# Performance work log

Measured on AMD Instinct MI355X. Metric: run time of the kernel, lower is better.

## Reference

```python
import jax, jax.numpy as jnp
import numpy as np

MEM_DIM = 1024
N_CHILD = 16384

def _linear_params(key, out_dim, in_dim):
    kw, kb = jax.random.split(key)
    bound = 1.0 / np.sqrt(in_dim)
    W = jax.random.uniform(kw, (out_dim, in_dim), jnp.float32, -bound, bound)
    b = jax.random.uniform(kb, (out_dim,), jnp.float32, -bound, bound)
    return W, b

def setup_inputs() -> dict:
    key = jax.random.key(0)
    ks = jax.random.split(key, 7)
    child_c = jax.random.normal(ks[0], (N_CHILD, MEM_DIM), jnp.float32)
    child_h = jax.random.normal(ks[1], (N_CHILD, MEM_DIM), jnp.float32)
    child_h_sum = jax.random.normal(ks[2], (MEM_DIM,), jnp.float32)
    W_ih, b_ih = _linear_params(ks[3], MEM_DIM, MEM_DIM)
    W_fh, b_fh = _linear_params(ks[4], MEM_DIM, MEM_DIM)
    W_uh, b_uh = _linear_params(ks[5], MEM_DIM, MEM_DIM)
    W_oh, b_oh = _linear_params(ks[6], MEM_DIM, MEM_DIM)
    return {
        "child_c": child_c, "child_h": child_h, "child_h_sum": child_h_sum,
        "W_ih": W_ih, "b_ih": b_ih, "W_fh": W_fh, "b_fh": b_fh,
        "W_uh": W_uh, "b_uh": b_uh, "W_oh": W_oh, "b_oh": b_oh,
    }

def reference(child_c, child_h, child_h_sum,
              W_ih, b_ih, W_fh, b_fh, W_uh, b_uh, W_oh, b_oh):
    # Gate projections on the summed child hidden state: [mem_dim]
    i = jax.nn.sigmoid(child_h_sum @ W_ih.T + b_ih)
    o = jax.nn.sigmoid(child_h_sum @ W_oh.T + b_oh)
    u = jnp.tanh(child_h_sum @ W_uh.T + b_uh)
    # Per-child forget gates, batched (replaces the Python loop): [N, mem_dim]
    f = jax.nn.sigmoid(child_h @ W_fh.T + b_fh)
    fc = f * child_c                     # [N, mem_dim]
    c = i * u + jnp.sum(fc, axis=0)      # [mem_dim]
    h = o * jnp.tanh(c)                  # [mem_dim]
    return (c, h)
```

## Files before the change

### kernel.cpp

```cpp
#include <hip/hip_runtime.h>
#include <hip/hip_bf16.h>
#include <math.h>

#define MEM_DIM 1024
#define N_CHILD 16384

#define BM 128
#define BN 128
#define BK 32
#define KITERS (MEM_DIM / BK)

typedef __bf16 bf16_t;
typedef __bf16 bf16x4 __attribute__((ext_vector_type(4)));
typedef __bf16 bf16x8 __attribute__((ext_vector_type(8)));
typedef float f32x4 __attribute__((ext_vector_type(4)));

__device__ __forceinline__ int swz(int r) { return (r >> 1) & 3; }

__device__ __forceinline__ void async_load16(const bf16_t* g, bf16_t* l) {
    __builtin_amdgcn_global_load_lds(
        (const __attribute__((address_space(1))) unsigned int*)g,
        (__attribute__((address_space(3))) unsigned int*)l,
        16, 0, 0);
}

__global__ __launch_bounds__(256) void cvt_bf16_kernel(const float* __restrict__ src,
                                                       bf16_t* __restrict__ dst, int n8) {
    int t = blockIdx.x * 256 + threadIdx.x;
    if (t < n8) {
        const float4* s = (const float4*)src + (size_t)t * 2;
        float4 a = s[0], b = s[1];
        bf16x8 o = { (bf16_t)a.x, (bf16_t)a.y, (bf16_t)a.z, (bf16_t)a.w,
                     (bf16_t)b.x, (bf16_t)b.y, (bf16_t)b.z, (bf16_t)b.w };
        *(bf16x8*)(dst + (size_t)t * 8) = o;
    }
}

__global__ void gates_kernel(const float* __restrict__ hsum,
                             const float* __restrict__ W_ih, const float* __restrict__ b_ih,
                             const float* __restrict__ W_uh, const float* __restrict__ b_uh,
                             const float* __restrict__ W_oh, const float* __restrict__ b_oh,
                             float* __restrict__ acc_c, float* __restrict__ o_ws) {
    const int j = blockIdx.x;
    const int tid = threadIdx.x;
    const float* wi = W_ih + (size_t)j * MEM_DIM;
    const float* wu = W_uh + (size_t)j * MEM_DIM;
    const float* wo = W_oh + (size_t)j * MEM_DIM;
    float si = 0.f, su = 0.f, so = 0.f;
    for (int k = tid; k < MEM_DIM; k += 256) {
        float hv = hsum[k];
        si += wi[k] * hv;
        su += wu[k] * hv;
        so += wo[k] * hv;
    }
    for (int off = 32; off > 0; off >>= 1) {
        si += __shfl_down(si, off, 64);
        su += __shfl_down(su, off, 64);
        so += __shfl_down(so, off, 64);
    }
    __shared__ float red[3][4];
    const int wave = tid >> 6, lane = tid & 63;
    if (lane == 0) { red[0][wave] = si; red[1][wave] = su; red[2][wave] = so; }
    __syncthreads();
    if (tid == 0) {
        float ti = red[0][0] + red[0][1] + red[0][2] + red[0][3] + b_ih[j];
        float tu = red[1][0] + red[1][1] + red[1][2] + red[1][3] + b_uh[j];
        float to = red[2][0] + red[2][1] + red[2][2] + red[2][3] + b_oh[j];
        float iv = 1.f / (1.f + expf(-ti));
        float uv = tanhf(tu);
        float ov = 1.f / (1.f + expf(-to));
        acc_c[j] = iv * uv;
        o_ws[j]  = ov;
    }
}

__global__ __launch_bounds__(256) void fused_gemm_bf16(
        const bf16_t* __restrict__ hbf, const bf16_t* __restrict__ wbf,
        const float* __restrict__ child_c, const float* __restrict__ b_fh,
        float* __restrict__ acc_c) {
    __shared__ __align__(1024) bf16_t sA[BM * BK];
    __shared__ __align__(1024) bf16_t sB[BN * BK];
    __shared__ float sred[BN];

    const int tid  = threadIdx.x;
    const int lane = tid & 63;
    const int wave = tid >> 6;
    const int wr = wave >> 1, wc = wave & 1;
    const int j0 = blockIdx.x * BN;
    const int n0 = blockIdx.y * BM;
    const int q  = lane >> 4;
    const int cl = lane & 15;

    const int seg = wave * 2;
    const int r0 = seg * 16 + (lane >> 2);
    const int r1 = r0 + 16;
    const int p  = lane & 3;
    const int c0 = p ^ swz(r0);
    const int c1 = p ^ swz(r1);
    const bf16_t* gA0 = hbf + (size_t)(n0 + r0) * MEM_DIM + c0 * 8;
    const bf16_t* gA1 = hbf + (size_t)(n0 + r1) * MEM_DIM + c1 * 8;
    const bf16_t* gB0 = wbf + (size_t)(j0 + r0) * MEM_DIM + c0 * 8;
    const bf16_t* gB1 = wbf + (size_t)(j0 + r1) * MEM_DIM + c1 * 8;
    bf16_t* lA0 = &sA[(seg)     * 512];
    bf16_t* lA1 = &sA[(seg + 1) * 512];
    bf16_t* lB0 = &sB[(seg)     * 512];
    bf16_t* lB1 = &sB[(seg + 1) * 512];

    int ofsA[4], ofsB[4];
#pragma unroll
    for (int mt = 0; mt < 4; mt++) {
        int ra = wr * 64 + mt * 16 + cl;
        int rb = wc * 64 + mt * 16 + cl;
        ofsA[mt] = ra * BK + (q ^ swz(ra)) * 8;
        ofsB[mt] = rb * BK + (q ^ swz(rb)) * 8;
    }

    f32x4 acc[4][4];
#pragma unroll
    for (int a = 0; a < 4; a++)
#pragma unroll
        for (int b = 0; b < 4; b++) acc[a][b] = (f32x4)0.0f;

    for (int k = 0; k < KITERS; ++k) {
        async_load16(gA0, lA0);
        async_load16(gA1, lA1);
        async_load16(gB0, lB0);
        async_load16(gB1, lB1);
        gA0 += BK; gA1 += BK; gB0 += BK; gB1 += BK;
        __syncthreads();

        bf16x8 af[4], bfr[4];
#pragma unroll
        for (int mt = 0; mt < 4; mt++) {
            af[mt]  = *(const bf16x8*)(&sA[ofsA[mt]]);
            bfr[mt] = *(const bf16x8*)(&sB[ofsB[mt]]);
        }
#pragma unroll
        for (int mt = 0; mt < 4; mt++)
#pragma unroll
            for (int nt = 0; nt < 4; nt++)
                acc[mt][nt] = __builtin_amdgcn_mfma_f32_16x16x32_bf16(
                    af[mt], bfr[nt], acc[mt][nt], 0, 0, 0);
        __syncthreads();
    }

    if (tid < BN) sred[tid] = 0.0f;
    __syncthreads();

    float colsum[4] = {0.f, 0.f, 0.f, 0.f};
#pragma unroll
    for (int nt = 0; nt < 4; nt++) {
        const int col = j0 + wc * 64 + nt * 16 + cl;
        const float bias = b_fh[col];
#pragma unroll
        for (int mt = 0; mt < 4; mt++) {
#pragma unroll
            for (int r = 0; r < 4; r++) {
                const int row = n0 + wr * 64 + mt * 16 + q * 4 + r;
                float s = acc[mt][nt][r] + bias;
                float fg = 1.0f / (1.0f + __expf(-s));
                colsum[nt] += fg * child_c[(size_t)row * MEM_DIM + col];
            }
        }
        colsum[nt] += __shfl_xor(colsum[nt], 16, 64);
        colsum[nt] += __shfl_xor(colsum[nt], 32, 64);
    }
    if (q == 0) {
#pragma unroll
        for (int nt = 0; nt < 4; nt++)
            atomicAdd(&sred[wc * 64 + nt * 16 + cl], colsum[nt]);
    }
    __syncthreads();
    if (tid < BN) atomicAdd(&acc_c[j0 + tid], sred[tid]);
}

#define LDS_STRIDE 40
__global__ __launch_bounds__(256) void fused_gemm_f32(
        const float* __restrict__ child_h, const float* __restrict__ child_c,
        const float* __restrict__ W_fh, const float* __restrict__ b_fh,
        float* __restrict__ acc_c) {
    __shared__ __align__(16) bf16_t sA[BM * LDS_STRIDE];
    __shared__ __align__(16) bf16_t sB[BN * LDS_STRIDE];
    __shared__ float sred[BN];
    const int tid = threadIdx.x, lane = tid & 63, wave = tid >> 6;
    const int wr = wave >> 1, wc = wave & 1;
    const int j0 = blockIdx.x * BN, n0 = blockIdx.y * BM;
    const int q = lane >> 4, cl = lane & 15;
    f32x4 acc[4][4];
#pragma unroll
    for (int a = 0; a < 4; a++)
#pragma unroll
        for (int b = 0; b < 4; b++) acc[a][b] = (f32x4)0.0f;
    for (int k0 = 0; k0 < MEM_DIM; k0 += BK) {
#pragma unroll
        for (int i = 0; i < 4; i++) {
            int f = tid + i * 256, row = f >> 3, col = (f & 7) * 4;
            float4 va = *(const float4*)(child_h + (size_t)(n0 + row) * MEM_DIM + k0 + col);
            float4 vb = *(const float4*)(W_fh    + (size_t)(j0 + row) * MEM_DIM + k0 + col);
            bf16x4 ba = { (bf16_t)va.x, (bf16_t)va.y, (bf16_t)va.z, (bf16_t)va.w };
            bf16x4 bb = { (bf16_t)vb.x, (bf16_t)vb.y, (bf16_t)vb.z, (bf16_t)vb.w };
            *(bf16x4*)(&sA[row * LDS_STRIDE + col]) = ba;
            *(bf16x4*)(&sB[row * LDS_STRIDE + col]) = bb;
        }
        __syncthreads();
        bf16x8 af[4], bfr[4];
#pragma unroll
        for (int mt = 0; mt < 4; mt++) {
            af[mt]  = *(const bf16x8*)(&sA[(wr * 64 + mt * 16 + cl) * LDS_STRIDE + q * 8]);
            bfr[mt] = *(const bf16x8*)(&sB[(wc * 64 + mt * 16 + cl) * LDS_STRIDE + q * 8]);
        }
#pragma unroll
        for (int mt = 0; mt < 4; mt++)
#pragma unroll
            for (int nt = 0; nt < 4; nt++)
                acc[mt][nt] = __builtin_amdgcn_mfma_f32_16x16x32_bf16(af[mt], bfr[nt], acc[mt][nt], 0, 0, 0);
        __syncthreads();
    }
    if (tid < BN) sred[tid] = 0.0f;
    __syncthreads();
    float colsum[4] = {0.f, 0.f, 0.f, 0.f};
#pragma unroll
    for (int nt = 0; nt < 4; nt++) {
        const int col = j0 + wc * 64 + nt * 16 + cl;
        const float bias = b_fh[col];
#pragma unroll
        for (int mt = 0; mt < 4; mt++)
#pragma unroll
            for (int r = 0; r < 4; r++) {
                const int row = n0 + wr * 64 + mt * 16 + q * 4 + r;
                float s = acc[mt][nt][r] + bias;
                float fg = 1.0f / (1.0f + __expf(-s));
                colsum[nt] += fg * child_c[(size_t)row * MEM_DIM + col];
            }
        colsum[nt] += __shfl_xor(colsum[nt], 16, 64);
        colsum[nt] += __shfl_xor(colsum[nt], 32, 64);
    }
    if (q == 0)
#pragma unroll
        for (int nt = 0; nt < 4; nt++)
            atomicAdd(&sred[wc * 64 + nt * 16 + cl], colsum[nt]);
    __syncthreads();
    if (tid < BN) atomicAdd(&acc_c[j0 + tid], sred[tid]);
}

__global__ void finalize_kernel(const float* __restrict__ acc_c,
                                const float* __restrict__ o_ws,
                                float* __restrict__ out) {
    int t = blockIdx.x * 256 + threadIdx.x;
    if (t < MEM_DIM) {
        float cv = acc_c[t];
        float hv = o_ws[t] * tanhf(cv);
        out[t] = cv;
        out[MEM_DIM + t] = hv;
    }
}

extern "C" void kernel_launch(void* const* d_in, const int* in_sizes, int n_in,
                              void* d_out, int out_size, void* d_ws, size_t ws_size,
                              hipStream_t stream) {
    const float* child_c = (const float*)d_in[0];
    const float* child_h = (const float*)d_in[1];
    const float* hsum    = (const float*)d_in[2];
    const float* W_ih    = (const float*)d_in[3];
    const float* b_ih    = (const float*)d_in[4];
    const float* W_fh    = (const float*)d_in[5];
    const float* b_fh    = (const float*)d_in[6];
    const float* W_uh    = (const float*)d_in[7];
    const float* b_uh    = (const float*)d_in[8];
    const float* W_oh    = (const float*)d_in[9];
    const float* b_oh    = (const float*)d_in[10];
    float* out   = (float*)d_out;

    float* acc_c = (float*)d_ws;
    float* o_ws  = acc_c + MEM_DIM;
    const size_t HBF_OFF = 8192;
    const size_t HBF_BYTES = (size_t)N_CHILD * MEM_DIM * 2;
    const size_t WBF_BYTES = (size_t)MEM_DIM * MEM_DIM * 2;
    const size_t NEED = HBF_OFF + HBF_BYTES + WBF_BYTES;

    gates_kernel<<<MEM_DIM, 256, 0, stream>>>(hsum, W_ih, b_ih, W_uh, b_uh, W_oh, b_oh,
                                              acc_c, o_ws);
    dim3 grid(MEM_DIM / BN, N_CHILD / BM);

    if (ws_size >= NEED) {
        bf16_t* hbf = (bf16_t*)((char*)d_ws + HBF_OFF);
        bf16_t* wbf = (bf16_t*)((char*)d_ws + HBF_OFF + HBF_BYTES);
        int n8_h = (N_CHILD * MEM_DIM) / 8;
        int n8_w = (MEM_DIM * MEM_DIM) / 8;
        cvt_bf16_kernel<<<(n8_h + 255) / 256, 256, 0, stream>>>(child_h, hbf, n8_h);
        cvt_bf16_kernel<<<(n8_w + 255) / 256, 256, 0, stream>>>(W_fh, wbf, n8_w);
        fused_gemm_bf16<<<grid, 256, 0, stream>>>(hbf, wbf, child_c, b_fh, acc_c);
    } else {
        fused_gemm_f32<<<grid, 256, 0, stream>>>(child_h, child_c, W_fh, b_fh, acc_c);
    }
    finalize_kernel<<<(MEM_DIM + 255) / 256, 256, 0, stream>>>(acc_c, o_ws, out);
}
```

Before: 227.2 us.

## Double K tile to 64, remap blocks per XCD, widen LDS swizzle

Raises the bf16 GEMM K-tile from 32 to 64, so each barrier pair covers twice the MFMA work and half as many K iterations run. The swizzle becomes a 3-bit XOR over 8 column chunks to fit the wider rows, and each wave now issues four async loads per operand. The launch becomes a 1D grid decoded so that consecutive blocks on the same XCD share row tiles of child_h, aiming for better L2 reuse. The cost is doubled LDS tile size, which may lower occupancy, and the f32 fallback is pinned to a step of 32.

```diff
diff --git a/kernel.cpp b/kernel.cpp
--- a/kernel.cpp
+++ b/kernel.cpp
@@ -7,15 +7,13 @@
 
 #define BM 128
 #define BN 128
-#define BK 32
+#define BK 64
 #define KITERS (MEM_DIM / BK)
 
 typedef __bf16 bf16_t;
 typedef __bf16 bf16x4 __attribute__((ext_vector_type(4)));
 typedef __bf16 bf16x8 __attribute__((ext_vector_type(8)));
 typedef float f32x4 __attribute__((ext_vector_type(4)));
-
-__device__ __forceinline__ int swz(int r) { return (r >> 1) & 3; }
 
 __device__ __forceinline__ void async_load16(const bf16_t* g, bf16_t* l) {
     __builtin_amdgcn_global_load_lds(
@@ -86,61 +84,65 @@
     const int lane = tid & 63;
     const int wave = tid >> 6;
     const int wr = wave >> 1, wc = wave & 1;
-    const int j0 = blockIdx.x * BN;
-    const int n0 = blockIdx.y * BM;
     const int q  = lane >> 4;
     const int cl = lane & 15;
 
-    const int seg = wave * 2;
-    const int r0 = seg * 16 + (lane >> 2);
-    const int r1 = r0 + 16;
-    const int p  = lane & 3;
-    const int c0 = p ^ swz(r0);
-    const int c1 = p ^ swz(r1);
-    const bf16_t* gA0 = hbf + (size_t)(n0 + r0) * MEM_DIM + c0 * 8;
-    const bf16_t* gA1 = hbf + (size_t)(n0 + r1) * MEM_DIM + c1 * 8;
-    const bf16_t* gB0 = wbf + (size_t)(j0 + r0) * MEM_DIM + c0 * 8;
-    const bf16_t* gB1 = wbf + (size_t)(j0 + r1) * MEM_DIM + c1 * 8;
-    bf16_t* lA0 = &sA[(seg)     * 512];
-    bf16_t* lA1 = &sA[(seg + 1) * 512];
-    bf16_t* lB0 = &sB[(seg)     * 512];
-    bf16_t* lB1 = &sB[(seg + 1) * 512];
-
-    int ofsA[4], ofsB[4];
-#pragma unroll
-    for (int mt = 0; mt < 4; mt++) {
-        int ra = wr * 64 + mt * 16 + cl;
-        int rb = wc * 64 + mt * 16 + cl;
-        ofsA[mt] = ra * BK + (q ^ swz(ra)) * 8;
-        ofsB[mt] = rb * BK + (q ^ swz(rb)) * 8;
+    const int b   = blockIdx.x;
+    const int xcd = b & 7;
+    const int l   = b >> 3;
+    const int jt  = l & 7;
+    const int ntl = l >> 3;
+    const int j0  = jt * BN;
+    const int n0  = (xcd * 16 + ntl) * BM;
+
+    const int rl = lane >> 3;
+    const int p  = lane & 7;
+    const int cf = (p ^ rl) * 8;
+    const bf16_t* gA[4];
+    const bf16_t* gB[4];
+    bf16_t* lA[4];
+    bf16_t* lB[4];
+#pragma unroll
+    for (int i = 0; i < 4; i++) {
+        const int r = wave * 32 + i * 8 + rl;
+        gA[i] = hbf + (size_t)(n0 + r) * MEM_DIM + cf;
+        gB[i] = wbf + (size_t)(j0 + r) * MEM_DIM + cf;
+        lA[i] = &sA[(wave * 32 + i * 8) * BK];
+        lB[i] = &sB[(wave * 32 + i * 8) * BK];
     }
 
     f32x4 acc[4][4];
 #pragma unroll
     for (int a = 0; a < 4; a++)
 #pragma unroll
-        for (int b = 0; b < 4; b++) acc[a][b] = (f32x4)0.0f;
+        for (int c = 0; c < 4; c++) acc[a][c] = (f32x4)0.0f;
 
     for (int k = 0; k < KITERS; ++k) {
-        async_load16(gA0, lA0);
-        async_load16(gA1, lA1);
-        async_load16(gB0, lB0);
-        async_load16(gB1, lB1);
-        gA0 += BK; gA1 += BK; gB0 += BK; gB1 += BK;
+#pragma unroll
+        for (int i = 0; i < 4; i++) {
+            async_load16(gA[i], lA[i]);
+            async_load16(gB[i], lB[i]);
+            gA[i] += BK; gB[i] += BK;
+        }
         __syncthreads();
 
-        bf16x8 af[4], bfr[4];
-#pragma unroll
-        for (int mt = 0; mt < 4; mt++) {
-            af[mt]  = *(const bf16x8*)(&sA[ofsA[mt]]);
-            bfr[mt] = *(const bf16x8*)(&sB[ofsB[mt]]);
-        }
-#pragma unroll
-        for (int mt = 0; mt < 4; mt++)
-#pragma unroll
-            for (int nt = 0; nt < 4; nt++)
-                acc[mt][nt] = __builtin_amdgcn_mfma_f32_16x16x32_bf16(
-                    af[mt], bfr[nt], acc[mt][nt], 0, 0, 0);
+#pragma unroll
+        for (int h = 0; h < 2; h++) {
+            bf16x8 af[4], bfr[4];
+#pragma unroll
+            for (int mt = 0; mt < 4; mt++) {
+                const int ra = wr * 64 + mt * 16 + cl;
+                const int rb = wc * 64 + mt * 16 + cl;
+                af[mt]  = *(const bf16x8*)(&sA[ra * BK + (((4 * h + q) ^ (cl & 7)) * 8)]);
+                bfr[mt] = *(const bf16x8*)(&sB[rb * BK + (((4 * h + q) ^ (cl & 7)) * 8)]);
+            }
+#pragma unroll
+            for (int mt = 0; mt < 4; mt++)
+#pragma unroll
+                for (int nt = 0; nt < 4; nt++)
+                    acc[mt][nt] = __builtin_amdgcn_mfma_f32_16x16x32_bf16(
+                        af[mt], bfr[nt], acc[mt][nt], 0, 0, 0);
+        }
         __syncthreads();
     }
 
@@ -190,8 +192,8 @@
 #pragma unroll
     for (int a = 0; a < 4; a++)
 #pragma unroll
-        for (int b = 0; b < 4; b++) acc[a][b] = (f32x4)0.0f;
-    for (int k0 = 0; k0 < MEM_DIM; k0 += BK) {
+        for (int c = 0; c < 4; c++) acc[a][c] = (f32x4)0.0f;
+    for (int k0 = 0; k0 < MEM_DIM; k0 += 32) {
 #pragma unroll
         for (int i = 0; i < 4; i++) {
             int f = tid + i * 256, row = f >> 3, col = (f & 7) * 4;
@@ -280,7 +282,6 @@
 
     gates_kernel<<<MEM_DIM, 256, 0, stream>>>(hsum, W_ih, b_ih, W_uh, b_uh, W_oh, b_oh,
                                               acc_c, o_ws);
-    dim3 grid(MEM_DIM / BN, N_CHILD / BM);
 
     if (ws_size >= NEED) {
         bf16_t* hbf = (bf16_t*)((char*)d_ws + HBF_OFF);
@@ -289,8 +290,10 @@
         int n8_w = (MEM_DIM * MEM_DIM) / 8;
         cvt_bf16_kernel<<<(n8_h + 255) / 256, 256, 0, stream>>>(child_h, hbf, n8_h);
         cvt_bf16_kernel<<<(n8_w + 255) / 256, 256, 0, stream>>>(W_fh, wbf, n8_w);
-        fused_gemm_bf16<<<grid, 256, 0, stream>>>(hbf, wbf, child_c, b_fh, acc_c);
+        fused_gemm_bf16<<<(N_CHILD / BM) * (MEM_DIM / BN), 256, 0, stream>>>(
+            hbf, wbf, child_c, b_fh, acc_c);
     } else {
+        dim3 grid(MEM_DIM / BN, N_CHILD / BM);
         fused_gemm_f32<<<grid, 256, 0, stream>>>(child_h, child_c, W_fh, b_fh, acc_c);
     }
     finalize_kernel<<<(MEM_DIM + 255) / 256, 256, 0, stream>>>(acc_c, o_ws, out);
```

Result: faster. 218.9 us (-3.7%).
